# Kernel optimization log

Hardware: AMD Instinct MI355X
Metric: run time of the kernel (lower is better)

Reference implementation:

```python
import jax, jax.numpy as jnp
import numpy as np

THRESHOLD = 1.0
BETA = 0.9  # initial mem is zeros, so mem = beta*0 + u = u


def spike(u):
    # forward of SurrogateGradient: (u > threshold).float()
    return (u > THRESHOLD).astype(u.dtype)


def rope_tables(seq_len, head_dim, base=10000.0):
    inv_freq = 1.0 / (base ** (jnp.arange(0, head_dim, 2, dtype=jnp.float32) / head_dim))
    t = jnp.arange(seq_len, dtype=jnp.float32)
    freqs = jnp.einsum('i,j->ij', t, inv_freq)          # [S, d/2]
    emb = jnp.concatenate([freqs, freqs], axis=-1)       # [S, d]
    return jnp.cos(emb), jnp.sin(emb)


def apply_rope(x, cos, sin):
    # x: [B, S, H, d]
    x1, x2 = jnp.split(x, 2, axis=-1)
    rot = jnp.concatenate([-x2, x1], axis=-1)
    return x * cos[None, :, None, :] + rot * sin[None, :, None, :]


def setup_inputs() -> dict:
    key = jax.random.key(0)
    ks = jax.random.split(key, 5)
    B, S, D = 1, 2048, 2048
    std = 1.0 / np.sqrt(D)
    return {
        'x':  jax.random.normal(ks[0], (B, S, D), jnp.float32),
        'Wq': jax.random.normal(ks[1], (D, D), jnp.float32) * std,
        'Wk': jax.random.normal(ks[2], (D, D), jnp.float32) * std,
        'Wv': jax.random.normal(ks[3], (D, D), jnp.float32) * std,
        'Wo': jax.random.normal(ks[4], (D, D), jnp.float32) * std,
    }


def reference(x, Wq, Wk, Wv, Wo):
    B, S, D = x.shape
    H, hd = 16, 128
    scale = hd ** -0.5

    q = (x @ Wq).reshape(B, S, H, hd)
    k = (x @ Wk).reshape(B, S, H, hd)
    v = (x @ Wv).reshape(B, S, H, hd)

    # LIF: mem starts at zero -> mem = q; spike = (mem > threshold)
    sq, sk, sv = spike(q), spike(k), spike(v)

    cos, sin = rope_tables(S, hd)
    rq = apply_rope(sq, cos, sin)
    rk = apply_rope(sk, cos, sin)

    scores = jnp.einsum('bqhd,bkhd->bhqk', rq, rk) * scale  # [B,H,S,S]
    causal = jnp.tril(jnp.ones((S, S), dtype=bool))
    scores = jnp.where(causal[None, None], scores, -jnp.inf)
    attn = jax.nn.softmax(scores, axis=-1)

    out = jnp.einsum('bhqk,bkhd->bqhd', attn, sv).reshape(B, S, H * hd)
    return out @ Wo
```

## Files before the change

kernel.cpp:

```cpp
#include <hip/hip_runtime.h>

typedef unsigned short u16;
typedef unsigned int u32;
typedef u16 u16x4 __attribute__((ext_vector_type(4)));
typedef u16 u16x8 __attribute__((ext_vector_type(8)));
typedef float f32x4 __attribute__((ext_vector_type(4)));
typedef __bf16 bf16x8 __attribute__((ext_vector_type(8)));
typedef _Float16 f16x4 __attribute__((ext_vector_type(4)));
typedef _Float16 f16x8 __attribute__((ext_vector_type(8)));

#define DD 2048
#define SCALE_ATTN 0.08838834764831845f
#define DELTA 0.005f

#define GL16(g, l)                                                              \
  __builtin_amdgcn_global_load_lds((const __attribute__((address_space(1))) u32*)(g), \
                                   (__attribute__((address_space(3))) u32*)(l), 16, 0, 0)

__device__ __forceinline__ u16 f2bf(float f) {
  u32 u = __float_as_uint(f);
  u32 r = (u + 0x7FFFu + ((u >> 16) & 1u)) >> 16;
  return (u16)r;
}
__device__ __forceinline__ float bf2f(u16 h) { return __uint_as_float(((u32)h) << 16); }

__global__ void k_prep(const float* __restrict__ x, _Float16* __restrict__ xf,
                       float* __restrict__ cosT, float* __restrict__ sinT,
                       const float* __restrict__ Wq, const float* __restrict__ Wk,
                       const float* __restrict__ Wv, const float* __restrict__ Wo,
                       _Float16* __restrict__ Wq16, _Float16* __restrict__ Wk16,
                       _Float16* __restrict__ Wv16, float* __restrict__ Wq32,
                       float* __restrict__ Wk32, float* __restrict__ Wv32,
                       u16* __restrict__ BoT) {
  __shared__ float tile[32][33];
  int y = blockIdx.y;
  if (y == 0) {
    int gi = blockIdx.x * 256 + threadIdx.x;
    int i = gi * 4;
    float4 v = *(const float4*)&x[i];
    f16x4 o = {(_Float16)v.x, (_Float16)v.y, (_Float16)v.z, (_Float16)v.w};
    *(f16x4*)&xf[i] = o;
    if (gi < 131072) {
      int s = gi >> 6, j = gi & 63;
      float e = (float)(2 * j) / 128.0f;
      float inv = 1.0f / powf(10000.0f, e);
      float fr = (float)s * inv;
      cosT[gi] = cosf(fr);
      sinT[gi] = sinf(fr);
    }
    return;
  }
  int m = y - 1;
  const float* W = m == 0 ? Wq : (m == 1 ? Wk : (m == 2 ? Wv : Wo));
  int bk = blockIdx.x & 63, bn = blockIdx.x >> 6;
  int c = threadIdx.x & 31, r0 = threadIdx.x >> 5;
#pragma unroll
  for (int i = 0; i < 4; ++i) {
    int r = r0 + i * 8;
    tile[r][c] = W[(size_t)(bk * 32 + r) * DD + bn * 32 + c];
  }
  __syncthreads();
  if (m < 3) {
    _Float16* WT16 = m == 0 ? Wq16 : (m == 1 ? Wk16 : Wv16);
    float* WT32 = m == 0 ? Wq32 : (m == 1 ? Wk32 : Wv32);
#pragma unroll
    for (int i = 0; i < 4; ++i) {
      int r = r0 + i * 8;
      float v = tile[c][r];
      size_t o = (size_t)(bn * 32 + r) * DD + bk * 32 + c;
      WT16[o] = (_Float16)v;
      WT32[o] = v;
    }
  } else {
#pragma unroll
    for (int i = 0; i < 4; ++i) {
      int r = r0 + i * 8;
      BoT[(size_t)(bn * 32 + r) * DD + bk * 32 + c] = f2bf(tile[c][r]);
    }
  }
}

__global__ void k_post(u16* sq, u16* sk, const float* __restrict__ cosT,
                       const float* __restrict__ sinT, const u16* __restrict__ sv,
                       u16* __restrict__ svT) {
  __shared__ u16 tile[32][33];
  int bid = blockIdx.x;
  if (bid < 8192) {
    int i = bid * 256 + threadIdx.x;
    int s = i >> 10;
    int rest = i & 1023;
    int h = rest >> 6, j = rest & 63;
    size_t base = (size_t)s * DD + h * 128 + j;
    float c = cosT[(s << 6) | j], sn = sinT[(s << 6) | j];
    float a = bf2f(sq[base]), b = bf2f(sq[base + 64]);
    sq[base] = f2bf(a * c - b * sn);
    sq[base + 64] = f2bf(b * c + a * sn);
    a = bf2f(sk[base]);
    b = bf2f(sk[base + 64]);
    sk[base] = f2bf(a * c - b * sn);
    sk[base + 64] = f2bf(b * c + a * sn);
  } else {
    int b = bid - 8192;
    int bk = b & 63, bn = b >> 6;
    int c = threadIdx.x & 31, r0 = threadIdx.x >> 5;
#pragma unroll
    for (int i = 0; i < 4; ++i) {
      int r = r0 + i * 8;
      tile[r][c] = sv[(size_t)(bk * 32 + r) * DD + bn * 32 + c];
    }
    __syncthreads();
#pragma unroll
    for (int i = 0; i < 4; ++i) {
      int r = r0 + i * 8;
      svT[(size_t)(bn * 32 + r) * DD + bk * 32 + c] = tile[c][r];
    }
  }
}

__global__ __launch_bounds__(256) void k_gemm_qkv(
    const _Float16* __restrict__ xf, const _Float16* __restrict__ BqT,
    const _Float16* __restrict__ BkT, const _Float16* __restrict__ BvT, u16* __restrict__ Sq,
    u16* __restrict__ Sk, u16* __restrict__ Sv, unsigned char* __restrict__ flagT) {
  __shared__ u16 lA[2 * 4096];
  __shared__ u16 lB[2 * 4096];

  const _Float16* BT = blockIdx.y == 0 ? BqT : (blockIdx.y == 1 ? BkT : BvT);
  u16* Out = blockIdx.y == 0 ? Sq : (blockIdx.y == 1 ? Sk : Sv);
  unsigned char* flT = flagT + (size_t)blockIdx.y * 4194304;

  int bid = blockIdx.x;
  int swz = (bid & 7) * 32 + (bid >> 3);
  int m0 = (swz >> 4) * 128, n0 = (swz & 15) * 128;

  int tid = threadIdx.x;
  int lane = tid & 63;
  int w = tid >> 6;
  int wr = (w >> 1) * 64, wc = (w & 1) * 64;
  int l15 = lane & 15, g8 = (lane >> 4) * 8;

  int ar0 = tid >> 2, ac0 = (tid & 3) << 3;
  int ar1 = (tid + 256) >> 2, ac1 = (tid & 3) << 3;

  f32x4 zero = {0.f, 0.f, 0.f, 0.f};
  f32x4 acc[4][4];
#pragma unroll
  for (int i = 0; i < 4; ++i)
#pragma unroll
    for (int j = 0; j < 4; ++j) acc[i][j] = zero;

  u16* laBase0 = lA + w * 512;
  u16* laBase1 = lA + 2048 + w * 512;
  u16* lbBase0 = lB + w * 512;
  u16* lbBase1 = lB + 2048 + w * 512;

  auto stage = [&](int buf, int vs) {
    int k0 = vs << 5;
    int bo = buf * 4096;
    GL16(&xf[(size_t)(m0 + ar0) * DD + k0 + ac0], laBase0 + bo);
    GL16(&xf[(size_t)(m0 + ar1) * DD + k0 + ac1], laBase1 + bo);
    GL16(&BT[(size_t)(n0 + ar0) * DD + k0 + ac0], lbBase0 + bo);
    GL16(&BT[(size_t)(n0 + ar1) * DD + k0 + ac1], lbBase1 + bo);
  };

  stage(0, 0);
  __syncthreads();
  for (int vs = 0; vs < 64; ++vs) {
    int cur = vs & 1;
    if (vs + 1 < 64) stage(cur ^ 1, vs + 1);
    const u16* la = lA + cur * 4096;
    const u16* lb = lB + cur * 4096;
    f16x8 af[4], bfr[4];
#pragma unroll
    for (int i = 0; i < 4; ++i) af[i] = *(const f16x8*)&la[(wr + i * 16 + l15) * 32 + g8];
#pragma unroll
    for (int j = 0; j < 4; ++j) bfr[j] = *(const f16x8*)&lb[(wc + j * 16 + l15) * 32 + g8];
#pragma unroll
    for (int i = 0; i < 4; ++i)
#pragma unroll
      for (int j = 0; j < 4; ++j)
        acc[i][j] = __builtin_amdgcn_mfma_f32_16x16x32_f16(af[i], bfr[j], acc[i][j], 0, 0, 0);
    __syncthreads();
  }

  int g4 = (lane >> 4) * 4;
#pragma unroll
  for (int i = 0; i < 4; ++i) {
    int row0 = m0 + wr + i * 16 + g4;
#pragma unroll
    for (int j = 0; j < 4; ++j) {
      int col = n0 + wc + j * 16 + l15;
      u32 fw = 0;
#pragma unroll
      for (int r = 0; r < 4; ++r) {
        float u = acc[i][j][r];
        Out[(size_t)(row0 + r) * DD + col] = (u > 1.0f) ? (u16)0x3F80 : (u16)0;
        if (fabsf(u - 1.0f) < DELTA) fw |= (1u << (8 * r));
      }
      *(u32*)&flT[(size_t)col * 2048 + row0] = fw;
    }
  }
}

__global__ __launch_bounds__(256) void k_fixup(
    const float* __restrict__ x, const float* __restrict__ WqT, const float* __restrict__ WkT,
    const float* __restrict__ WvT, const unsigned char* __restrict__ flagT,
    u16* __restrict__ Sq, u16* __restrict__ Sk, u16* __restrict__ Sv) {
  __shared__ u32 lw[256];
  __shared__ u32 wsum[4];
  __shared__ u32 lcnt;
  int tid = threadIdx.x;
  int lane = tid & 63;
  int w = tid >> 6;
  size_t blockBase = (size_t)blockIdx.x * 16384;
  const u32* fp = (const u32*)(flagT + blockBase);
  unsigned long long fm = 0;
#pragma unroll
  for (int it = 0; it < 4; ++it) {
    u32 m16 = 0;
#pragma unroll
    for (int wd = 0; wd < 4; ++wd) {
      u32 v = fp[it * 1024 + tid * 4 + wd];
      m16 |= (((v >> 0) & 1u) | ((v >> 7) & 2u) | ((v >> 14) & 4u) | ((v >> 21) & 8u)) << (wd * 4);
    }
    fm |= (unsigned long long)m16 << (it * 16);
  }
  u32 c = (u32)__popcll(fm);
  u32 pre = c;
#pragma unroll
  for (int d = 1; d < 64; d <<= 1) {
    u32 t = __shfl_up(pre, d, 64);
    if (lane >= d) pre += t;
  }
  if (lane == 63) wsum[w] = pre;
  __syncthreads();
  u32 wbase = 0;
#pragma unroll
  for (int i = 0; i < 4; ++i)
    if (i < w) wbase += wsum[i];
  if (tid == 0) {
    u32 tot = wsum[0] + wsum[1] + wsum[2] + wsum[3];
    lcnt = tot > 256u ? 256u : tot;
  }
  u32 pos = wbase + pre - c;
  while (fm) {
    int p = __ffsll((long long)fm) - 1;
    fm &= fm - 1;
    u32 e = (u32)blockBase + (u32)(p >> 4) * 4096u + (u32)tid * 16u + (u32)(p & 15);
    if (pos < 256u) lw[pos] = e;
    ++pos;
  }
  __syncthreads();
  u32 cnt = lcnt;
  for (u32 i = w; i < cnt; i += 4) {
    u32 e = lw[i];
    int ii = (int)(e & 2047u);
    int j = (int)((e >> 11) & 2047u);
    int mat = (int)(e >> 22);
    const float* WT = mat == 0 ? WqT : (mat == 1 ? WkT : WvT);
    const float* xr = x + (size_t)ii * DD;
    const float* wrw = WT + (size_t)j * DD;
    float u = 0.f;
#pragma unroll
    for (int t = 0; t < 8; ++t) {
      float4 a = *(const float4*)&xr[t * 256 + lane * 4];
      float4 bv = *(const float4*)&wrw[t * 256 + lane * 4];
      u = fmaf(a.x, bv.x, u);
      u = fmaf(a.y, bv.y, u);
      u = fmaf(a.z, bv.z, u);
      u = fmaf(a.w, bv.w, u);
    }
#pragma unroll
    for (int sh = 32; sh; sh >>= 1) u += __shfl_xor(u, sh);
    if (lane == 0) {
      u16* Out2 = mat == 0 ? Sq : (mat == 1 ? Sk : Sv);
      Out2[(size_t)ii * DD + j] = (u > 1.0f) ? (u16)0x3F80 : (u16)0;
    }
  }
}

__global__ __launch_bounds__(256) void k_gemm_out(const u16* __restrict__ A,
                                                  const u16* __restrict__ BT,
                                                  float* __restrict__ C) {
  __shared__ u16 lA[2 * 4096];
  __shared__ u16 lB[2 * 2048];
  int bid = blockIdx.x;
  int swz = (bid & 7) * 64 + (bid >> 3);
  int m0 = (swz >> 5) * 128, n0 = (swz & 31) * 64;
  int tid = threadIdx.x;
  int lane = tid & 63;
  int w = tid >> 6;
  int wr = (w >> 1) * 64, wc = (w & 1) * 32;
  int l15 = lane & 15, g8 = (lane >> 4) * 8;
  int ar0 = tid >> 2, ac = (tid & 3) << 3;
  int ar1 = ar0 + 64;
  f32x4 zero = {0.f, 0.f, 0.f, 0.f};
  f32x4 acc[4][2];
#pragma unroll
  for (int i = 0; i < 4; ++i)
#pragma unroll
    for (int j = 0; j < 2; ++j) acc[i][j] = zero;

  u16* laBase0 = lA + w * 512;
  u16* laBase1 = lA + 2048 + w * 512;
  u16* lbBase = lB + w * 512;

  auto stage = [&](int buf, int vs) {
    int k0 = vs << 5;
    GL16(&A[(size_t)(m0 + ar0) * DD + k0 + ac], laBase0 + buf * 4096);
    GL16(&A[(size_t)(m0 + ar1) * DD + k0 + ac], laBase1 + buf * 4096);
    GL16(&BT[(size_t)(n0 + ar0) * DD + k0 + ac], lbBase + buf * 2048);
  };

  stage(0, 0);
  __syncthreads();
  for (int vs = 0; vs < 64; ++vs) {
    int cur = vs & 1;
    if (vs + 1 < 64) stage(cur ^ 1, vs + 1);
    const u16* la = lA + cur * 4096;
    const u16* lb = lB + cur * 2048;
    bf16x8 af[4], bfr[2];
#pragma unroll
    for (int i = 0; i < 4; ++i) af[i] = *(const bf16x8*)&la[(wr + i * 16 + l15) * 32 + g8];
#pragma unroll
    for (int j = 0; j < 2; ++j) bfr[j] = *(const bf16x8*)&lb[(wc + j * 16 + l15) * 32 + g8];
#pragma unroll
    for (int i = 0; i < 4; ++i)
#pragma unroll
      for (int j = 0; j < 2; ++j)
        acc[i][j] = __builtin_amdgcn_mfma_f32_16x16x32_bf16(af[i], bfr[j], acc[i][j], 0, 0, 0);
    __syncthreads();
  }

  int g4 = (lane >> 4) * 4;
#pragma unroll
  for (int i = 0; i < 4; ++i) {
    int row0 = m0 + wr + i * 16 + g4;
#pragma unroll
    for (int j = 0; j < 2; ++j) {
      int col = n0 + wc + j * 16 + l15;
#pragma unroll
      for (int r = 0; r < 4; ++r) C[(size_t)(row0 + r) * DD + col] = acc[i][j][r];
    }
  }
}

__global__ __launch_bounds__(256) void k_attn(const u16* __restrict__ rq,
                                              const u16* __restrict__ rk,
                                              const u16* __restrict__ svT,
                                              u16* __restrict__ outp) {
  __shared__ u16 lrk[64 * 136];
  __shared__ u16 lsv[128 * 72];
  __shared__ u16 lP[4 * 16 * 72];

  int bid = blockIdx.x;
  int h = bid & 15;
  int i0 = bid >> 4;
  int qb = 31 - i0;
  int q0 = qb * 64;

  int tid = threadIdx.x;
  int lane = tid & 63;
  int w = tid >> 6;
  int l15 = lane & 15;
  int g = lane >> 4;
  int qw = q0 + w * 16;
  int qpos = qw + l15;
  int pb = w * 1152 + l15 * 72;

  bf16x8 rqf[4];
#pragma unroll
  for (int ks = 0; ks < 4; ++ks)
    rqf[ks] = *(const bf16x8*)&rq[(size_t)qpos * DD + h * 128 + ks * 32 + g * 8];

  f32x4 zero = {0.f, 0.f, 0.f, 0.f};
  f32x4 acc[8];
#pragma unroll
  for (int dt = 0; dt < 8; ++dt) acc[dt] = zero;
  float mrun = -1e30f, lrun = 0.f;

  u16x8 sk_[4], sv_[4];
  auto issue = [&](int t) {
    int kv0 = t << 6;
#pragma unroll
    for (int p = 0; p < 4; ++p) {
      int idx = tid + p * 256;
      int r = idx >> 4, c8 = (idx & 15) << 3;
      sk_[p] = *(const u16x8*)&rk[(size_t)(kv0 + r) * DD + h * 128 + c8];
      int r2 = idx >> 3, d8 = (idx & 7) << 3;
      sv_[p] = *(const u16x8*)&svT[(size_t)(h * 128 + r2) * DD + kv0 + d8];
    }
  };

  int nt = (q0 >> 6) + 1;
  issue(0);
  for (int t = 0; t < nt; ++t) {
    int kv0 = t << 6;
    __syncthreads();
#pragma unroll
    for (int p = 0; p < 4; ++p) {
      int idx = tid + p * 256;
      int r = idx >> 4, c8 = (idx & 15) << 3;
      *(u16x8*)&lrk[r * 136 + c8] = sk_[p];
      int r2 = idx >> 3, d8 = (idx & 7) << 3;
      *(u16x8*)&lsv[r2 * 72 + d8] = sv_[p];
    }
    __syncthreads();
    if (t + 1 < nt) issue(t + 1);

    f32x4 sacc[4];
#pragma unroll
    for (int kt = 0; kt < 4; ++kt) sacc[kt] = zero;
    __builtin_amdgcn_s_setprio(1);
#pragma unroll
    for (int kt = 0; kt < 4; ++kt)
#pragma unroll
      for (int ks = 0; ks < 4; ++ks) {
        bf16x8 a = *(const bf16x8*)&lrk[(kt * 16 + l15) * 136 + ks * 32 + g * 8];
        sacc[kt] = __builtin_amdgcn_mfma_f32_16x16x32_bf16(a, rqf[ks], sacc[kt], 0, 0, 0);
      }
    __builtin_amdgcn_s_setprio(0);
    float p[4][4];
    float mx = -1e30f;
#pragma unroll
    for (int kt = 0; kt < 4; ++kt)
#pragma unroll
      for (int rr = 0; rr < 4; ++rr) {
        int kvpos = kv0 + kt * 16 + g * 4 + rr;
        float sc = sacc[kt][rr] * SCALE_ATTN;
        sc = (kvpos <= qpos) ? sc : -1e30f;
        p[kt][rr] = sc;
        mx = fmaxf(mx, sc);
      }
    mx = fmaxf(mx, __shfl_xor(mx, 16));
    mx = fmaxf(mx, __shfl_xor(mx, 32));
    float mnew = fmaxf(mrun, mx);
    float alpha = __expf(mrun - mnew);
    float rs = 0.f;
#pragma unroll
    for (int kt = 0; kt < 4; ++kt)
#pragma unroll
      for (int rr = 0; rr < 4; ++rr) {
        float e = __expf(p[kt][rr] - mnew);
        p[kt][rr] = e;
        rs += e;
      }
    rs += __shfl_xor(rs, 16);
    rs += __shfl_xor(rs, 32);
    lrun = lrun * alpha + rs;
    mrun = mnew;
    float al[4];
#pragma unroll
    for (int rr = 0; rr < 4; ++rr) al[rr] = __shfl(alpha, (lane & 48) | (g * 4 + rr), 64);
#pragma unroll
    for (int dt = 0; dt < 8; ++dt)
#pragma unroll
      for (int rr = 0; rr < 4; ++rr) acc[dt][rr] *= al[rr];
#pragma unroll
    for (int kt = 0; kt < 4; ++kt) {
      u16x4 pk = {f2bf(p[kt][0]), f2bf(p[kt][1]), f2bf(p[kt][2]), f2bf(p[kt][3])};
      *(u16x4*)&lP[pb + kt * 16 + g * 4] = pk;
    }
    bf16x8 pa0 = *(const bf16x8*)&lP[pb + g * 8];
    bf16x8 pa1 = *(const bf16x8*)&lP[pb + 32 + g * 8];
    __builtin_amdgcn_s_setprio(1);
#pragma unroll
    for (int dt = 0; dt < 8; ++dt) {
      bf16x8 b0 = *(const bf16x8*)&lsv[(dt * 16 + l15) * 72 + g * 8];
      acc[dt] = __builtin_amdgcn_mfma_f32_16x16x32_bf16(pa0, b0, acc[dt], 0, 0, 0);
      bf16x8 b1 = *(const bf16x8*)&lsv[(dt * 16 + l15) * 72 + 32 + g * 8];
      acc[dt] = __builtin_amdgcn_mfma_f32_16x16x32_bf16(pa1, b1, acc[dt], 0, 0, 0);
    }
    __builtin_amdgcn_s_setprio(0);
  }

  float linv[4];
#pragma unroll
  for (int rr = 0; rr < 4; ++rr)
    linv[rr] = 1.0f / __shfl(lrun, (lane & 48) | (g * 4 + rr), 64);
#pragma unroll
  for (int dt = 0; dt < 8; ++dt)
#pragma unroll
    for (int rr = 0; rr < 4; ++rr) {
      int row = qw + g * 4 + rr;
      outp[(size_t)row * DD + h * 128 + dt * 16 + l15] = f2bf(acc[dt][rr] * linv[rr]);
    }
}

extern "C" void kernel_launch(void* const* d_in, const int* in_sizes, int n_in, void* d_out,
                              int out_size, void* d_ws, size_t ws_size, hipStream_t stream) {
  (void)in_sizes;
  (void)n_in;
  (void)out_size;
  const float* x = (const float*)d_in[0];
  const float* Wq = (const float*)d_in[1];
  const float* Wk = (const float*)d_in[2];
  const float* Wv = (const float*)d_in[3];
  const float* Wo = (const float*)d_in[4];
  float* out = (float*)d_out;

  const size_t SZ = (size_t)DD * DD;
  size_t need = 35 * SZ + 2 * (size_t)2048 * 64 * 4;
  if (ws_size < need) return;

  char* p = (char*)d_ws;
  auto a2 = [&](void) {
    void* q = (void*)p;
    p += SZ * 2;
    return q;
  };
  _Float16* xf = (_Float16*)a2();
  _Float16* WqT16 = (_Float16*)a2();
  _Float16* WkT16 = (_Float16*)a2();
  _Float16* WvT16 = (_Float16*)a2();
  u16* BoT = (u16*)a2();
  u16* sq = (u16*)a2();
  u16* sk = (u16*)a2();
  u16* sv = (u16*)a2();
  u16* svT = (u16*)a2();
  u16* outp = (u16*)a2();
  float* WqT32 = (float*)p;
  p += SZ * 4;
  float* WkT32 = (float*)p;
  p += SZ * 4;
  float* WvT32 = (float*)p;
  p += SZ * 4;
  unsigned char* flagT = (unsigned char*)p;
  p += 3 * SZ;
  float* cosT = (float*)p;
  p += (size_t)2048 * 64 * 4;
  float* sinT = (float*)p;

  k_prep<<<dim3(4096, 5, 1), 256, 0, stream>>>(x, xf, cosT, sinT, Wq, Wk, Wv, Wo, WqT16, WkT16,
                                               WvT16, WqT32, WkT32, WvT32, BoT);
  k_gemm_qkv<<<dim3(256, 3, 1), 256, 0, stream>>>(xf, WqT16, WkT16, WvT16, sq, sk, sv, flagT);
  k_fixup<<<768, 256, 0, stream>>>(x, WqT32, WkT32, WvT32, flagT, sq, sk, sv);
  k_post<<<12288, 256, 0, stream>>>(sq, sk, cosT, sinT, sv, svT);
  k_attn<<<512, 256, 0, stream>>>(sq, sk, svT, outp);
  k_gemm_out<<<512, 256, 0, stream>>>(outp, BoT, out);
}
```

Measured before the change: 273.1 us.

## Fuse RoPE and V transpose into attention kernel, drop post-processing pass

Removes the separate k_post kernel that applied RoPE to q/k in place and transposed v. The attention kernel now applies RoPE to q at load and to each k tile while staging into LDS, and transposes v through scalar LDS stores with a padded stride of 74. Cos/sin tables are stored as bf16 to halve their traffic. This saves a kernel launch and a full read/write pass over q, k and v, at the cost of redundant RoPE work on k across query blocks and more scattered LDS stores. Rounding the cos/sin tables to bf16 adds a small precision loss.

```diff
diff --git a/kernel.cpp b/kernel.cpp
--- a/kernel.cpp
+++ b/kernel.cpp
@@ -25,7 +25,7 @@
 __device__ __forceinline__ float bf2f(u16 h) { return __uint_as_float(((u32)h) << 16); }
 
 __global__ void k_prep(const float* __restrict__ x, _Float16* __restrict__ xf,
-                       float* __restrict__ cosT, float* __restrict__ sinT,
+                       u16* __restrict__ cosB, u16* __restrict__ sinB,
                        const float* __restrict__ Wq, const float* __restrict__ Wk,
                        const float* __restrict__ Wv, const float* __restrict__ Wo,
                        _Float16* __restrict__ Wq16, _Float16* __restrict__ Wk16,
@@ -45,8 +45,8 @@
       float e = (float)(2 * j) / 128.0f;
       float inv = 1.0f / powf(10000.0f, e);
       float fr = (float)s * inv;
-      cosT[gi] = cosf(fr);
-      sinT[gi] = sinf(fr);
+      cosB[gi] = f2bf(cosf(fr));
+      sinB[gi] = f2bf(sinf(fr));
     }
     return;
   }
@@ -76,43 +76,6 @@
     for (int i = 0; i < 4; ++i) {
       int r = r0 + i * 8;
       BoT[(size_t)(bn * 32 + r) * DD + bk * 32 + c] = f2bf(tile[c][r]);
-    }
-  }
-}
-
-__global__ void k_post(u16* sq, u16* sk, const float* __restrict__ cosT,
-                       const float* __restrict__ sinT, const u16* __restrict__ sv,
-                       u16* __restrict__ svT) {
-  __shared__ u16 tile[32][33];
-  int bid = blockIdx.x;
-  if (bid < 8192) {
-    int i = bid * 256 + threadIdx.x;
-    int s = i >> 10;
-    int rest = i & 1023;
-    int h = rest >> 6, j = rest & 63;
-    size_t base = (size_t)s * DD + h * 128 + j;
-    float c = cosT[(s << 6) | j], sn = sinT[(s << 6) | j];
-    float a = bf2f(sq[base]), b = bf2f(sq[base + 64]);
-    sq[base] = f2bf(a * c - b * sn);
-    sq[base + 64] = f2bf(b * c + a * sn);
-    a = bf2f(sk[base]);
-    b = bf2f(sk[base + 64]);
-    sk[base] = f2bf(a * c - b * sn);
-    sk[base + 64] = f2bf(b * c + a * sn);
-  } else {
-    int b = bid - 8192;
-    int bk = b & 63, bn = b >> 6;
-    int c = threadIdx.x & 31, r0 = threadIdx.x >> 5;
-#pragma unroll
-    for (int i = 0; i < 4; ++i) {
-      int r = r0 + i * 8;
-      tile[r][c] = sv[(size_t)(bk * 32 + r) * DD + bn * 32 + c];
-    }
-    __syncthreads();
-#pragma unroll
-    for (int i = 0; i < 4; ++i) {
-      int r = r0 + i * 8;
-      svT[(size_t)(bn * 32 + r) * DD + bk * 32 + c] = tile[c][r];
     }
   }
 }
@@ -344,12 +307,14 @@
   }
 }
 
-__global__ __launch_bounds__(256) void k_attn(const u16* __restrict__ rq,
-                                              const u16* __restrict__ rk,
-                                              const u16* __restrict__ svT,
+__global__ __launch_bounds__(256) void k_attn(const u16* __restrict__ sq,
+                                              const u16* __restrict__ sk,
+                                              const u16* __restrict__ sv,
+                                              const u16* __restrict__ cosB,
+                                              const u16* __restrict__ sinB,
                                               u16* __restrict__ outp) {
   __shared__ u16 lrk[64 * 136];
-  __shared__ u16 lsv[128 * 72];
+  __shared__ u16 lsv[128 * 74];
   __shared__ u16 lP[4 * 16 * 72];
 
   int bid = blockIdx.x;
@@ -368,9 +333,27 @@
   int pb = w * 1152 + l15 * 72;
 
   bf16x8 rqf[4];
-#pragma unroll
-  for (int ks = 0; ks < 4; ++ks)
-    rqf[ks] = *(const bf16x8*)&rq[(size_t)qpos * DD + h * 128 + ks * 32 + g * 8];
+  {
+    u16x8 raw[4];
+#pragma unroll
+    for (int ks = 0; ks < 4; ++ks)
+      raw[ks] = *(const u16x8*)&sq[(size_t)qpos * DD + h * 128 + ks * 32 + g * 8];
+#pragma unroll
+    for (int ks = 0; ks < 2; ++ks) {
+      u16x8 cb = *(const u16x8*)&cosB[(qpos << 6) + ks * 32 + g * 8];
+      u16x8 sb = *(const u16x8*)&sinB[(qpos << 6) + ks * 32 + g * 8];
+      u16x8 lo, hi;
+#pragma unroll
+      for (int e = 0; e < 8; ++e) {
+        float a = bf2f(raw[ks][e]), b = bf2f(raw[ks + 2][e]);
+        float c = bf2f(cb[e]), s = bf2f(sb[e]);
+        lo[e] = f2bf(a * c - b * s);
+        hi[e] = f2bf(b * c + a * s);
+      }
+      rqf[ks] = __builtin_bit_cast(bf16x8, lo);
+      rqf[ks + 2] = __builtin_bit_cast(bf16x8, hi);
+    }
+  }
 
   f32x4 zero = {0.f, 0.f, 0.f, 0.f};
   f32x4 acc[8];
@@ -378,16 +361,21 @@
   for (int dt = 0; dt < 8; ++dt) acc[dt] = zero;
   float mrun = -1e30f, lrun = 0.f;
 
-  u16x8 sk_[4], sv_[4];
+  u16x4 klo_[4], khi_[4], kc_[4], ksn_[4];
+  u16x8 sv_[4];
   auto issue = [&](int t) {
     int kv0 = t << 6;
 #pragma unroll
     for (int p = 0; p < 4; ++p) {
       int idx = tid + p * 256;
-      int r = idx >> 4, c8 = (idx & 15) << 3;
-      sk_[p] = *(const u16x8*)&rk[(size_t)(kv0 + r) * DD + h * 128 + c8];
-      int r2 = idx >> 3, d8 = (idx & 7) << 3;
-      sv_[p] = *(const u16x8*)&svT[(size_t)(h * 128 + r2) * DD + kv0 + d8];
+      int r = idx >> 4, g4 = idx & 15;
+      size_t kb = (size_t)(kv0 + r) * DD + h * 128 + g4 * 4;
+      klo_[p] = *(const u16x4*)&sk[kb];
+      khi_[p] = *(const u16x4*)&sk[kb + 64];
+      kc_[p] = *(const u16x4*)&cosB[((kv0 + r) << 6) + g4 * 4];
+      ksn_[p] = *(const u16x4*)&sinB[((kv0 + r) << 6) + g4 * 4];
+      int rv = idx >> 4, dv = (idx & 15) << 3;
+      sv_[p] = *(const u16x8*)&sv[(size_t)(kv0 + rv) * DD + h * 128 + dv];
     }
   };
 
@@ -399,10 +387,20 @@
 #pragma unroll
     for (int p = 0; p < 4; ++p) {
       int idx = tid + p * 256;
-      int r = idx >> 4, c8 = (idx & 15) << 3;
-      *(u16x8*)&lrk[r * 136 + c8] = sk_[p];
-      int r2 = idx >> 3, d8 = (idx & 7) << 3;
-      *(u16x8*)&lsv[r2 * 72 + d8] = sv_[p];
+      int r = idx >> 4, g4 = idx & 15;
+      u16x4 lo, hi;
+#pragma unroll
+      for (int e = 0; e < 4; ++e) {
+        float a = bf2f(klo_[p][e]), b = bf2f(khi_[p][e]);
+        float c = bf2f(kc_[p][e]), s = bf2f(ksn_[p][e]);
+        lo[e] = f2bf(a * c - b * s);
+        hi[e] = f2bf(b * c + a * s);
+      }
+      *(u16x4*)&lrk[r * 136 + g4 * 4] = lo;
+      *(u16x4*)&lrk[r * 136 + 64 + g4 * 4] = hi;
+      int rv = idx >> 4, dv = (idx & 15) << 3;
+#pragma unroll
+      for (int e = 0; e < 8; ++e) lsv[(dv + e) * 74 + rv] = sv_[p][e];
     }
     __syncthreads();
     if (t + 1 < nt) issue(t + 1);
@@ -465,9 +463,9 @@
     __builtin_amdgcn_s_setprio(1);
 #pragma unroll
     for (int dt = 0; dt < 8; ++dt) {
-      bf16x8 b0 = *(const bf16x8*)&lsv[(dt * 16 + l15) * 72 + g * 8];
+      bf16x8 b0 = *(const bf16x8*)&lsv[(dt * 16 + l15) * 74 + g * 8];
       acc[dt] = __builtin_amdgcn_mfma_f32_16x16x32_bf16(pa0, b0, acc[dt], 0, 0, 0);
-      bf16x8 b1 = *(const bf16x8*)&lsv[(dt * 16 + l15) * 72 + 32 + g * 8];
+      bf16x8 b1 = *(const bf16x8*)&lsv[(dt * 16 + l15) * 74 + 32 + g * 8];
       acc[dt] = __builtin_amdgcn_mfma_f32_16x16x32_bf16(pa1, b1, acc[dt], 0, 0, 0);
     }
     __builtin_amdgcn_s_setprio(0);
@@ -499,7 +497,7 @@
   float* out = (float*)d_out;
 
   const size_t SZ = (size_t)DD * DD;
-  size_t need = 35 * SZ + 2 * (size_t)2048 * 64 * 4;
+  size_t need = 33 * SZ + 2 * (size_t)2048 * 64 * 2;
   if (ws_size < need) return;
 
   char* p = (char*)d_ws;
@@ -516,7 +514,6 @@
   u16* sq = (u16*)a2();
   u16* sk = (u16*)a2();
   u16* sv = (u16*)a2();
-  u16* svT = (u16*)a2();
   u16* outp = (u16*)a2();
   float* WqT32 = (float*)p;
   p += SZ * 4;
@@ -526,15 +523,14 @@
   p += SZ * 4;
   unsigned char* flagT = (unsigned char*)p;
   p += 3 * SZ;
-  float* cosT = (float*)p;
-  p += (size_t)2048 * 64 * 4;
-  float* sinT = (float*)p;
-
-  k_prep<<<dim3(4096, 5, 1), 256, 0, stream>>>(x, xf, cosT, sinT, Wq, Wk, Wv, Wo, WqT16, WkT16,
+  u16* cosB = (u16*)p;
+  p += (size_t)2048 * 64 * 2;
+  u16* sinB = (u16*)p;
+
+  k_prep<<<dim3(4096, 5, 1), 256, 0, stream>>>(x, xf, cosB, sinB, Wq, Wk, Wv, Wo, WqT16, WkT16,
                                                WvT16, WqT32, WkT32, WvT32, BoT);
   k_gemm_qkv<<<dim3(256, 3, 1), 256, 0, stream>>>(xf, WqT16, WkT16, WvT16, sq, sk, sv, flagT);
   k_fixup<<<768, 256, 0, stream>>>(x, WqT32, WkT32, WvT32, flagT, sq, sk, sv);
-  k_post<<<12288, 256, 0, stream>>>(sq, sk, cosT, sinT, sv, svT);
-  k_attn<<<512, 256, 0, stream>>>(sq, sk, svT, outp);
+  k_attn<<<512, 256, 0, stream>>>(sq, sk, sv, cosB, sinB, outp);
   k_gemm_out<<<512, 256, 0, stream>>>(outp, BoT, out);
 }
```

Measured after the change: 302.6 us. +10.8%, slower.
